# Performance work log

Measured on AMD Instinct MI355X. Metric: run time of the kernel, lower is better.

Reference implementation:

```python
import jax, jax.numpy as jnp
import numpy as np

H = 2; C = 64          # heads, hidden_channels
N = 50000; E = 800000  # nodes, edges
D = 128                # input_dim
EPS = 1e-5

def _lrelu(x, s):
    return jnp.where(x >= 0, x, s * x)

def _ln(x, g, b):
    m = x.mean(-1, keepdims=True)
    v = ((x - m) ** 2).mean(-1, keepdims=True)
    return (x - m) / jnp.sqrt(v + EPS) * g + b

def _gatv2(x_src, x_dst, src, dst, Wl, bl, Wr, br, att, Wres, bias):
    # PyG GATv2Conv: concat=False (mean over heads), residual=True, no self loops
    n = x_dst.shape[0]
    xl = (x_src @ Wl + bl).reshape(-1, H, C)  # [Ns,H,C]
    xr = (x_dst @ Wr + br).reshape(-1, H, C)  # [Nd,H,C]
    xj = xl[src]                               # [E,H,C] messages from source
    xi = xr[dst]                               # [E,H,C]
    e = _lrelu(xi + xj, 0.2)
    alpha = jnp.einsum('ehc,hc->eh', e, att)   # [E,H]
    amax = jax.lax.stop_gradient(jax.ops.segment_max(alpha, dst, num_segments=n))
    ex = jnp.exp(alpha - amax[dst])
    den = jax.ops.segment_sum(ex, dst, num_segments=n)
    a = ex / den[dst]                          # segment softmax over incoming edges
    out = jax.ops.segment_sum(xj * a[:, :, None], dst, num_segments=n)  # [Nd,H,C]
    return out.mean(axis=1) + x_dst @ Wres + bias


def setup_inputs() -> dict:
    key = jax.random.key(0)
    ks = jax.random.split(key, 40)
    d = {}
    d['x'] = jax.random.normal(ks[0], (N, D), jnp.float32)
    d['edge_index'] = jax.random.randint(ks[1], (2, E), 0, N, jnp.int32)
    i = 2
    for p, ind in (('c1d', D), ('c1t', D), ('c2d', C), ('c2t', C)):
        d[p + '_Wl'] = jax.random.normal(ks[i], (ind, H * C), jnp.float32) * 0.05; i += 1
        d[p + '_bl'] = jnp.zeros((H * C,), jnp.float32)
        d[p + '_Wr'] = jax.random.normal(ks[i], (ind, H * C), jnp.float32) * 0.05; i += 1
        d[p + '_br'] = jnp.zeros((H * C,), jnp.float32)
        d[p + '_att'] = jax.random.normal(ks[i], (H, C), jnp.float32) * 0.05; i += 1
        d[p + '_Wres'] = jax.random.normal(ks[i], (ind, C), jnp.float32) * 0.05; i += 1
        d[p + '_bias'] = jnp.zeros((C,), jnp.float32)
    d['nd_g'] = jnp.ones((C,), jnp.float32); d['nd_b'] = jnp.zeros((C,), jnp.float32)
    d['nt_g'] = jnp.ones((C,), jnp.float32); d['nt_b'] = jnp.zeros((C,), jnp.float32)
    return d


def reference(x, edge_index, c1d_Wl, c1d_bl, c1d_Wr, c1d_br, c1d_att, c1d_Wres, c1d_bias, c1t_Wl, c1t_bl, c1t_Wr, c1t_br, c1t_att, c1t_Wres, c1t_bias, c2d_Wl, c2d_bl, c2d_Wr, c2d_br, c2d_att, c2d_Wres, c2d_bias, c2t_Wl, c2t_bl, c2t_Wr, c2t_br, c2t_att, c2t_Wres, c2t_bias, nd_g, nd_b, nt_g, nt_b):
    src, dst = edge_index[0], edge_index[1]
    dep = _gatv2(x, x, src, dst, c1d_Wl, c1d_bl, c1d_Wr, c1d_br, c1d_att, c1d_Wres, c1d_bias)
    dep = _lrelu(_ln(dep, nd_g, nd_b), 0.01)
    dant = _gatv2(x, x, dst, src, c1t_Wl, c1t_bl, c1t_Wr, c1t_br, c1t_att, c1t_Wres, c1t_bias)
    dant = _lrelu(_ln(dant, nt_g, nt_b), 0.01)
    dep2 = _lrelu(_gatv2(dep, dep, src, dst, c2d_Wl, c2d_bl, c2d_Wr, c2d_br, c2d_att, c2d_Wres, c2d_bias), 0.01)
    dant2 = _lrelu(_gatv2(dant, dant, dst, src, c2t_Wl, c2t_bl, c2t_Wr, c2t_br, c2t_att, c2t_Wres, c2t_bias), 0.01)
    return jnp.concatenate([dep2, dant2, x], axis=-1)
```

## Files before the change

### kernel.cpp

```cpp
#include <hip/hip_runtime.h>
#include <math.h>

typedef unsigned short ushort_t;
typedef __attribute__((ext_vector_type(8))) short short8x;
typedef __attribute__((ext_vector_type(4))) float f32x4;

#define SUBS 8
#define CAP 128

__device__ __forceinline__ unsigned f2bf(float f) {
  unsigned u = __float_as_uint(f);
  u += 0x7fff + ((u >> 16) & 1);
  return u >> 16;
}
__device__ __forceinline__ float bf2f(ushort_t u) {
  return __uint_as_float(((unsigned)u) << 16);
}
__device__ __forceinline__ float dpp_red8(float v) {
  v += __int_as_float(__builtin_amdgcn_update_dpp(0, __float_as_int(v), 0xB1, 0xF, 0xF, true));
  v += __int_as_float(__builtin_amdgcn_update_dpp(0, __float_as_int(v), 0x4E, 0xF, 0xF, true));
  v += __int_as_float(__builtin_amdgcn_update_dpp(0, __float_as_int(v), 0x141, 0xF, 0xF, true));
  return v;
}

struct GArgs {
  const float* Wl[2];
  const float* bl[2];
  const float* Wr[2];
  const float* br[2];
  const float* Wres[2];
  const float* bias[2];
};

__device__ __forceinline__ float wval1(const GArgs& ga, int col, int k) {
  int dir = col >= 320 ? 1 : 0;
  int cc = col - dir * 320;
  return cc < 128 ? ga.Wl[dir][k * 128 + cc]
       : cc < 256 ? ga.Wr[dir][k * 128 + (cc - 128)]
                  : ga.Wres[dir][k * 64 + (cc - 256)];
}
__device__ __forceinline__ float bval(const GArgs& ga, int col) {
  int dir = col >= 320 ? 1 : 0;
  int cc = col - dir * 320;
  return cc < 128 ? ga.bl[dir][cc]
       : cc < 256 ? ga.br[dir][cc - 128]
                  : ga.bias[dir][cc - 256];
}


__global__ __launch_bounds__(128) void pack_kernel(GArgs g1, GArgs g2,
                                                   ushort_t* __restrict__ WT1,
                                                   ushort_t* __restrict__ WT2,
                                                   float* __restrict__ bc1,
                                                   float* __restrict__ bc2) {
  int b = blockIdx.x;
  int k = threadIdx.x;
  if (b < 640) {
    WT1[b * 128 + k] = (ushort_t)f2bf(wval1(g1, b, k));
  } else if (b < 1280) {
    int c = b - 640;
    int dir = c >= 320 ? 1 : 0;
    int cc = c - dir * 320;
    float v = 0.f;
    if ((k >> 6) == dir) {
      int k2 = k & 63;
      v = cc < 128 ? g2.Wl[dir][k2 * 128 + cc]
        : cc < 256 ? g2.Wr[dir][k2 * 128 + (cc - 128)]
                   : g2.Wres[dir][k2 * 64 + (cc - 256)];
    }
    WT2[c * 128 + k] = (ushort_t)f2bf(v);
  } else {
    for (int c = k; c < 640; c += 128) {
      bc1[c] = bval(g1, c);
      bc2[c] = bval(g2, c);
    }
  }
}


template <int AF32>
__device__ __forceinline__ void gemm_body(const float* Af, const ushort_t* Ab,
                                          const ushort_t* WT, const float* bc,
                                          ushort_t* Y, int N, int rb, int cb,
                                          ushort_t* lds) {
  const int tid = threadIdx.x;
  const int lane = tid & 63;
  const int w = tid >> 6;
  const int m0 = rb * 64;
  const int cbase = cb * 128 + w * 32;

#pragma unroll
  for (int c = 0; c < 4; ++c) {
    int Lb = (tid + c * 256) * 16;
    int row = Lb >> 8, within = Lb & 255;
    int so = within ^ ((row & 7) << 4);
    int grow = m0 + row;
    if (grow >= N) grow = N - 1;
    if (AF32) {
      const float* src = Af + (size_t)grow * 128 + (so >> 1);
      float4 a = *(const float4*)src;
      float4 b = *(const float4*)(src + 4);
      uint4 o;
      o.x = f2bf(a.x) | (f2bf(a.y) << 16);
      o.y = f2bf(a.z) | (f2bf(a.w) << 16);
      o.z = f2bf(b.x) | (f2bf(b.y) << 16);
      o.w = f2bf(b.z) | (f2bf(b.w) << 16);
      ((uint4*)lds)[tid + c * 256] = o;
    } else {
      ((uint4*)lds)[tid + c * 256] = *(const uint4*)(Ab + (size_t)grow * 128 + (so >> 1));
    }
  }

  short8x bf[4][2];
#pragma unroll
  for (int ks = 0; ks < 4; ++ks)
#pragma unroll
    for (int ns = 0; ns < 2; ++ns) {
      int col = cbase + ns * 16 + (lane & 15);
      bf[ks][ns] = *(const short8x*)(WT + (size_t)col * 128 + ks * 32 + (lane >> 4) * 8);
    }

  __syncthreads();

  f32x4 z = {0.f, 0.f, 0.f, 0.f};
  f32x4 acc[4][2];
#pragma unroll
  for (int ms = 0; ms < 4; ++ms) {
    acc[ms][0] = z;
    acc[ms][1] = z;
  }
#pragma unroll
  for (int ks = 0; ks < 4; ++ks) {
    short8x af[4];
#pragma unroll
    for (int ms = 0; ms < 4; ++ms) {
      int row = ms * 16 + (lane & 15);
      int byte = row * 256 + ((ks * 64 + (lane >> 4) * 16) ^ ((row & 7) << 4));
      af[ms] = *(const short8x*)((const char*)lds + byte);
    }
#pragma unroll
    for (int ms = 0; ms < 4; ++ms) {
      acc[ms][0] = __builtin_amdgcn_mfma_f32_16x16x32_bf16(af[ms], bf[ks][0], acc[ms][0], 0, 0, 0);
      acc[ms][1] = __builtin_amdgcn_mfma_f32_16x16x32_bf16(af[ms], bf[ks][1], acc[ms][1], 0, 0, 0);
    }
  }

#pragma unroll
  for (int ms = 0; ms < 4; ++ms)
#pragma unroll
    for (int ns = 0; ns < 2; ++ns) {
      int col = cbase + ns * 16 + (lane & 15);
      float bv = bc[col];
#pragma unroll
      for (int r = 0; r < 4; ++r) {
        int grow = m0 + ms * 16 + (lane >> 4) * 4 + r;
        if (grow < N) Y[(size_t)grow * 640 + col] = (ushort_t)f2bf(acc[ms][ns][r] + bv);
      }
    }
}


__global__ __launch_bounds__(256) void k_front(
    const float* __restrict__ x, const int* __restrict__ ei, int E, int N,
    int* __restrict__ st0, int* __restrict__ st1, int* __restrict__ cnt0,
    int* __restrict__ cnt1, const ushort_t* __restrict__ WT1,
    const float* __restrict__ bc1, ushort_t* __restrict__ Y,
    float* __restrict__ out, int nbin, int ngemm, int nrow) {
  __shared__ ushort_t lds[8192];
  const int bid = blockIdx.x;
  const int t = threadIdx.x;
  if (bid < nbin) {
    const int sub = bid & (SUBS - 1);
    const int i0 = (bid * 256 + t) * 4;
    if (i0 >= E) return;
    if (i0 + 3 < E && (E & 3) == 0) {
      int4 sv = *(const int4*)(ei + i0);
      int4 dv = *(const int4*)(ei + E + i0);
      int ss[4] = {sv.x, sv.y, sv.z, sv.w};
      int dd[4] = {dv.x, dv.y, dv.z, dv.w};
      int pos[8], tgt[8];
#pragma unroll
      for (int j = 0; j < 4; ++j) {
        int c0 = (dd[j] >> 5) * SUBS + sub;
        tgt[j] = c0 * CAP;
        pos[j] = atomicAdd(&cnt0[c0], 1);
      }
#pragma unroll
      for (int j = 0; j < 4; ++j) {
        int c1 = (ss[j] >> 5) * SUBS + sub;
        tgt[4 + j] = c1 * CAP;
        pos[4 + j] = atomicAdd(&cnt1[c1], 1);
      }
#pragma unroll
      for (int j = 0; j < 4; ++j)
        if (pos[j] < CAP) st0[tgt[j] + pos[j]] = (ss[j] << 5) | (dd[j] & 31);
#pragma unroll
      for (int j = 0; j < 4; ++j)
        if (pos[4 + j] < CAP) st1[tgt[4 + j] + pos[4 + j]] = (dd[j] << 5) | (ss[j] & 31);
    } else {
      for (int i = i0; i < min(i0 + 4, E); ++i) {
        int s = ei[i], d = ei[E + i];
        int c0 = (d >> 5) * SUBS + sub;
        int i_ = atomicAdd(&cnt0[c0], 1);
        if (i_ < CAP) st0[c0 * CAP + i_] = (s << 5) | (d & 31);
        int c1 = (s >> 5) * SUBS + sub;
        int j_ = atomicAdd(&cnt1[c1], 1);
        if (j_ < CAP) st1[c1 * CAP + j_] = (d << 5) | (s & 31);
      }
    }
  } else if (bid < nbin + ngemm) {
    int gb = bid - nbin;
    gemm_body<1>(x, nullptr, WT1, bc1, Y, N, gb % nrow, gb / nrow, lds);
  } else {
    int i = (bid - nbin - ngemm) * 256 + t;
    if (i < N * 32) {
      float4 v = ((const float4*)x)[i];
      ((float4*)out)[(size_t)(i >> 5) * 64 + 32 + (i & 31)] = v;
    }
  }
}


__global__ __launch_bounds__(256) void gemm2_kernel(const ushort_t* __restrict__ A,
                                                    const ushort_t* __restrict__ WT,
                                                    const float* __restrict__ bc,
                                                    ushort_t* __restrict__ Y, int N) {
  __shared__ ushort_t lds[8192];
  gemm_body<0>(nullptr, A, WT, bc, Y, N, blockIdx.x, blockIdx.y, lds);
}


template <int MODE>
__global__ __launch_bounds__(256) void agg_bucket(
    const ushort_t* __restrict__ Y, const int* __restrict__ st0,
    const int* __restrict__ st1, const int* __restrict__ cnt0,
    const int* __restrict__ cnt1, const float* __restrict__ attA,
    const float* __restrict__ attB, const float* __restrict__ lng0,
    const float* __restrict__ lnb0, const float* __restrict__ lng1,
    const float* __restrict__ lnb1, void* __restrict__ outp, int N) {
  __shared__ int lnbr[SUBS * CAP + 8];
  __shared__ int hist[32], offs[32], cur[32];
  __shared__ int csub[SUBS + 1];
  const int b = blockIdx.x;
  const int dir = blockIdx.y;
  const int t = threadIdx.x;
  const int* st = dir ? st1 : st0;
  const int* cnt = dir ? cnt1 : cnt0;
  const float* att = dir ? attB : attA;

  for (int i = t; i < SUBS * CAP + 8; i += 256) lnbr[i] = 0;
  if (t < 32) {
    hist[t] = 0;
    cur[t] = 0;
  }
  if (t == 64) {
    int a = 0;
    for (int s = 0; s < SUBS; ++s) {
      csub[s] = a;
      a += min(cnt[b * SUBS + s], CAP);
    }
    csub[SUBS] = a;
  }
  __syncthreads();
#pragma unroll
  for (int s = 0; s < SUBS; ++s) {
    int base = csub[s], c = csub[s + 1] - base;
    for (int i = t; i < c; i += 256)
      atomicAdd(&hist[st[(b * SUBS + s) * CAP + i] & 31], 1);
  }
  __syncthreads();
  if (t < 32) {
    int v = hist[t], inc = v;
#pragma unroll
    for (int o = 1; o < 32; o <<= 1) {
      int u = __shfl_up(inc, o);
      if (t >= o) inc += u;
    }
    offs[t] = inc - v;
  }
  __syncthreads();
#pragma unroll
  for (int s = 0; s < SUBS; ++s) {
    int base = csub[s], c = csub[s + 1] - base;
    for (int i = t; i < c; i += 256) {
      int e = st[(b * SUBS + s) * CAP + i];
      int r = e & 31;
      lnbr[offs[r] + atomicAdd(&cur[r], 1)] = (int)((unsigned)e >> 5) * 1280;
    }
  }
  __syncthreads();

  const int wv = t >> 6, lane = t & 63, g = lane >> 4, jj = lane & 15;
  const float L2E = 1.4426950408889634f;
  float av[8];
  {
    float4 a0 = *(const float4*)(att + jj * 8);
    float4 a1 = *(const float4*)(att + jj * 8 + 4);
    av[0] = a0.x * L2E; av[1] = a0.y * L2E; av[2] = a0.z * L2E; av[3] = a0.w * L2E;
    av[4] = a1.x * L2E; av[5] = a1.y * L2E; av[6] = a1.z * L2E; av[7] = a1.w * L2E;
  }
  const char* Yb = (const char*)Y + dir * 640 + jj * 16;

  for (int r = wv; r < 32; r += 4) {
    const int n = b * 32 + r;
    if (n >= N) break;
    const char* rowp = (const char*)Y + (size_t)n * 1280 + dir * 640;

    float xi[8];
    {
      short8x v = *(const short8x*)(rowp + 256 + jj * 16);
#pragma unroll
      for (int q = 0; q < 8; ++q) xi[q] = bf2f((ushort_t)v[q]);
    }
    float d = 0.f;
    float acc[8];
#pragma unroll
    for (int q = 0; q < 8; ++q) acc[q] = 0.f;

    const int beg = offs[r], deg = hist[r];
    if (deg > 0) {
      int off = lnbr[beg + g];
      short8x vj = *(const short8x*)(Yb + (size_t)(unsigned)off);
      for (int k0 = 0; k0 < deg; k0 += 4) {
        int offn = lnbr[beg + k0 + 4 + g];
        short8x vn = *(const short8x*)(Yb + (size_t)(unsigned)offn);
        float xj[8];
#pragma unroll
        for (int q = 0; q < 8; ++q) xj[q] = bf2f((ushort_t)vj[q]);
        float p = 0.f;
#pragma unroll
        for (int q = 0; q < 8; ++q) {
          float e = xi[q] + xj[q];
          e = fmaxf(e, 0.2f * e);
          p = fmaf(e, av[q], p);
        }
        p = dpp_red8(p);
        float wgt = (k0 + g < deg) ? __builtin_amdgcn_exp2f(p) : 0.f;
        d += wgt;
#pragma unroll
        for (int q = 0; q < 8; ++q) acc[q] = fmaf(xj[q], wgt, acc[q]);
        vj = vn;
      }
#pragma unroll
      for (int o = 16; o <= 32; o <<= 1) {
        d += __shfl_xor(d, o);
#pragma unroll
        for (int q = 0; q < 8; ++q) acc[q] += __shfl_xor(acc[q], o);
      }
    }
    float inv = deg > 0 ? 1.f / d : 0.f;
    float v[8];
#pragma unroll
    for (int q = 0; q < 8; ++q) {
      float tq = acc[q] * inv;
      v[q] = 0.5f * (tq + __shfl_xor(tq, 8));
    }
    {
      short8x rv = *(const short8x*)(rowp + 512 + (jj & 7) * 16);
#pragma unroll
      for (int q = 0; q < 8; ++q) v[q] += bf2f((ushort_t)rv[q]);
    }

    if (MODE == 0) {
      float s = 0.f;
#pragma unroll
      for (int q = 0; q < 8; ++q) s += v[q];
      s += __shfl_xor(s, 1);
      s += __shfl_xor(s, 2);
      s += __shfl_xor(s, 4);
      float mu = s * (1.f / 64.f);
      float vs = 0.f;
#pragma unroll
      for (int q = 0; q < 8; ++q) {
        float dv = v[q] - mu;
        vs += dv * dv;
      }
      vs += __shfl_xor(vs, 1);
      vs += __shfl_xor(vs, 2);
      vs += __shfl_xor(vs, 4);
      float rstd = rsqrtf(vs * (1.f / 64.f) + 1e-5f);
      if (g == 0 && jj < 8) {
        const float* lg = dir ? lng1 : lng0;
        const float* lb = dir ? lnb1 : lnb0;
        unsigned o2[8];
#pragma unroll
        for (int q = 0; q < 8; ++q) {
          int c = jj * 8 + q;
          float y = (v[q] - mu) * rstd * lg[c] + lb[c];
          y = fmaxf(y, 0.01f * y);
          o2[q] = f2bf(y);
        }
        uint4 pk;
        pk.x = o2[0] | (o2[1] << 16);
        pk.y = o2[2] | (o2[3] << 16);
        pk.z = o2[4] | (o2[5] << 16);
        pk.w = o2[6] | (o2[7] << 16);
        *(uint4*)((ushort_t*)outp + (size_t)n * 128 + dir * 64 + jj * 8) = pk;
      }
    } else {
      if (g == 0 && jj < 8) {
        float* op = (float*)outp + (size_t)n * 256 + dir * 64 + jj * 8;
        float4 o0, o1;
        o0.x = fmaxf(v[0], 0.01f * v[0]);
        o0.y = fmaxf(v[1], 0.01f * v[1]);
        o0.z = fmaxf(v[2], 0.01f * v[2]);
        o0.w = fmaxf(v[3], 0.01f * v[3]);
        o1.x = fmaxf(v[4], 0.01f * v[4]);
        o1.y = fmaxf(v[5], 0.01f * v[5]);
        o1.z = fmaxf(v[6], 0.01f * v[6]);
        o1.w = fmaxf(v[7], 0.01f * v[7]);
        *(float4*)op = o0;
        *(float4*)(op + 4) = o1;
      }
    }
  }
}


extern "C" void kernel_launch(void* const* d_in, const int* in_sizes, int n_in,
                              void* d_out, int out_size, void* d_ws, size_t ws_size,
                              hipStream_t stream) {
  const float* x = (const float*)d_in[0];
  const int* ei = (const int*)d_in[1];
  const int N = in_sizes[0] / 128;
  const int E = in_sizes[1] / 2;
  float* out = (float*)d_out;
  const int nbuck = (N + 31) >> 5;

  char* p = (char*)d_ws;
  auto carve = [&](size_t bytes) {
    char* q = p;
    p += ((bytes + 255) & ~(size_t)255);
    return q;
  };
  int* cnt = (int*)carve((size_t)2 * nbuck * SUBS * 4);
  int* st0 = (int*)carve((size_t)nbuck * SUBS * CAP * 4);
  int* st1 = (int*)carve((size_t)nbuck * SUBS * CAP * 4);
  ushort_t* Y1 = (ushort_t*)carve((size_t)N * 640 * 2);
  ushort_t* A2 = (ushort_t*)carve((size_t)N * 128 * 2);
  ushort_t* WT1 = (ushort_t*)carve(640 * 128 * 2);
  ushort_t* WT2 = (ushort_t*)carve(640 * 128 * 2);
  float* bc1 = (float*)carve(640 * 4);
  float* bc2 = (float*)carve(640 * 4);
  int* cnt0 = cnt;
  int* cnt1 = cnt + (size_t)nbuck * SUBS;

  auto F = [&](int i) { return (const float*)d_in[i]; };
  GArgs g1, g2;
  g1.Wl[0] = F(2);  g1.bl[0] = F(3);  g1.Wr[0] = F(4);  g1.br[0] = F(5);
  g1.Wres[0] = F(7); g1.bias[0] = F(8);
  g1.Wl[1] = F(9);  g1.bl[1] = F(10); g1.Wr[1] = F(11); g1.br[1] = F(12);
  g1.Wres[1] = F(14); g1.bias[1] = F(15);
  g2.Wl[0] = F(16); g2.bl[0] = F(17); g2.Wr[0] = F(18); g2.br[0] = F(19);
  g2.Wres[0] = F(21); g2.bias[0] = F(22);
  g2.Wl[1] = F(23); g2.bl[1] = F(24); g2.Wr[1] = F(25); g2.br[1] = F(26);
  g2.Wres[1] = F(28); g2.bias[1] = F(29);

  hipMemsetAsync(cnt, 0, (size_t)2 * nbuck * SUBS * 4, stream);

  pack_kernel<<<1281, 128, 0, stream>>>(g1, g2, WT1, WT2, bc1, bc2);

  const int nbin = (E + 1023) / 1024;
  const int nrow = (N + 63) / 64;
  const int ngemm = nrow * 5;
  const int ncopy = (N * 32 + 255) / 256;
  k_front<<<nbin + ngemm + ncopy, 256, 0, stream>>>(
      x, ei, E, N, st0, st1, cnt0, cnt1, WT1, bc1, Y1, out, nbin, ngemm, nrow);

  const dim3 ga(nbuck, 2);
  agg_bucket<0><<<ga, 256, 0, stream>>>(Y1, st0, st1, cnt0, cnt1, F(6), F(13),
                                        F(30), F(31), F(32), F(33), A2, N);
  gemm2_kernel<<<dim3(nrow, 5), 256, 0, stream>>>(A2, WT2, bc2, Y1, N);
  agg_bucket<1><<<ga, 256, 0, stream>>>(Y1, st0, st1, cnt0, cnt1, F(20), F(27),
                                        nullptr, nullptr, nullptr, nullptr, out, N);
}
```

Before: 339.1 us.

## Replace fine-grained atomic edge binning with coarse LDS-histogram chunk binning

Edge binning now groups edges into 512-node coarse chunks. Each block builds LDS histograms and reserves space with one global atomic per chunk, instead of one global atomic per edge into 32-node sub-buckets. Aggregation blocks then scan their whole coarse chunk, filter the edges for their own 32 nodes into LDS, and sort them locally. This cuts contended global atomics in the front kernel. In exchange, each coarse chunk's edge list is read 16 times over in each aggregation pass, and endpoints are packed into 16-bit fields, which assumes fewer than 65536 nodes.

New measurement: 305.8 us. 1.11x faster.

```diff
diff --git a/kernel.cpp b/kernel.cpp
--- a/kernel.cpp
+++ b/kernel.cpp
@@ -5,8 +5,11 @@
 typedef __attribute__((ext_vector_type(8))) short short8x;
 typedef __attribute__((ext_vector_type(4))) float f32x4;
 
-#define SUBS 8
-#define CAP 128
+#define CSHIFT 9
+#define CC 12288
+#define EPB 4096
+#define ECAP 1024
+#define NCMAX 128
 
 __device__ __forceinline__ unsigned f2bf(float f) {
   unsigned u = __float_as_uint(f);
@@ -162,57 +165,53 @@
 
 __global__ __launch_bounds__(256) void k_front(
     const float* __restrict__ x, const int* __restrict__ ei, int E, int N,
-    int* __restrict__ st0, int* __restrict__ st1, int* __restrict__ cnt0,
-    int* __restrict__ cnt1, const ushort_t* __restrict__ WT1,
+    int* __restrict__ gc0, int* __restrict__ gc1, int* __restrict__ ctail0,
+    int* __restrict__ ctail1, const ushort_t* __restrict__ WT1,
     const float* __restrict__ bc1, ushort_t* __restrict__ Y,
-    float* __restrict__ out, int nbin, int ngemm, int nrow) {
+    float* __restrict__ out, int nbinA, int ngemm, int nrow) {
   __shared__ ushort_t lds[8192];
   const int bid = blockIdx.x;
   const int t = threadIdx.x;
-  if (bid < nbin) {
-    const int sub = bid & (SUBS - 1);
-    const int i0 = (bid * 256 + t) * 4;
-    if (i0 >= E) return;
-    if (i0 + 3 < E && (E & 3) == 0) {
-      int4 sv = *(const int4*)(ei + i0);
-      int4 dv = *(const int4*)(ei + E + i0);
-      int ss[4] = {sv.x, sv.y, sv.z, sv.w};
-      int dd[4] = {dv.x, dv.y, dv.z, dv.w};
-      int pos[8], tgt[8];
-#pragma unroll
-      for (int j = 0; j < 4; ++j) {
-        int c0 = (dd[j] >> 5) * SUBS + sub;
-        tgt[j] = c0 * CAP;
-        pos[j] = atomicAdd(&cnt0[c0], 1);
-      }
-#pragma unroll
-      for (int j = 0; j < 4; ++j) {
-        int c1 = (ss[j] >> 5) * SUBS + sub;
-        tgt[4 + j] = c1 * CAP;
-        pos[4 + j] = atomicAdd(&cnt1[c1], 1);
-      }
-#pragma unroll
-      for (int j = 0; j < 4; ++j)
-        if (pos[j] < CAP) st0[tgt[j] + pos[j]] = (ss[j] << 5) | (dd[j] & 31);
-#pragma unroll
-      for (int j = 0; j < 4; ++j)
-        if (pos[4 + j] < CAP) st1[tgt[4 + j] + pos[4 + j]] = (dd[j] << 5) | (ss[j] & 31);
-    } else {
-      for (int i = i0; i < min(i0 + 4, E); ++i) {
-        int s = ei[i], d = ei[E + i];
-        int c0 = (d >> 5) * SUBS + sub;
-        int i_ = atomicAdd(&cnt0[c0], 1);
-        if (i_ < CAP) st0[c0 * CAP + i_] = (s << 5) | (d & 31);
-        int c1 = (s >> 5) * SUBS + sub;
-        int j_ = atomicAdd(&cnt1[c1], 1);
-        if (j_ < CAP) st1[c1 * CAP + j_] = (d << 5) | (s & 31);
-      }
-    }
-  } else if (bid < nbin + ngemm) {
-    int gb = bid - nbin;
+  if (bid < nbinA) {
+    int* h0 = (int*)lds;
+    int* h1 = h0 + NCMAX;
+    int* b0 = h1 + NCMAX;
+    int* b1 = b0 + NCMAX;
+    const int e0 = bid * EPB;
+    const int e1 = min(e0 + EPB, E);
+    for (int i = t; i < NCMAX; i += 256) {
+      h0[i] = 0;
+      h1[i] = 0;
+    }
+    __syncthreads();
+    for (int i = e0 + t; i < e1; i += 256) {
+      int s = ei[i], d = ei[E + i];
+      atomicAdd(&h0[d >> CSHIFT], 1);
+      atomicAdd(&h1[s >> CSHIFT], 1);
+    }
+    __syncthreads();
+    for (int c = t; c < NCMAX; c += 256) {
+      int n0 = h0[c], n1 = h1[c];
+      b0[c] = n0 ? atomicAdd(&ctail0[c], n0) : 0;
+      b1[c] = n1 ? atomicAdd(&ctail1[c], n1) : 0;
+      h0[c] = 0;
+      h1[c] = 0;
+    }
+    __syncthreads();
+    for (int i = e0 + t; i < e1; i += 256) {
+      int s = ei[i], d = ei[E + i];
+      int c0 = d >> CSHIFT;
+      int p0 = b0[c0] + atomicAdd(&h0[c0], 1);
+      if (p0 < CC) gc0[c0 * CC + p0] = (s << 16) | d;
+      int c1 = s >> CSHIFT;
+      int p1 = b1[c1] + atomicAdd(&h1[c1], 1);
+      if (p1 < CC) gc1[c1 * CC + p1] = (d << 16) | s;
+    }
+  } else if (bid < nbinA + ngemm) {
+    int gb = bid - nbinA;
     gemm_body<1>(x, nullptr, WT1, bc1, Y, N, gb % nrow, gb / nrow, lds);
   } else {
-    int i = (bid - nbin - ngemm) * 256 + t;
+    int i = (bid - nbinA - ngemm) * 256 + t;
     if (i < N * 32) {
       float4 v = ((const float4*)x)[i];
       ((float4*)out)[(size_t)(i >> 5) * 64 + 32 + (i & 31)] = v;
@@ -232,42 +231,46 @@
 
 template <int MODE>
 __global__ __launch_bounds__(256) void agg_bucket(
-    const ushort_t* __restrict__ Y, const int* __restrict__ st0,
-    const int* __restrict__ st1, const int* __restrict__ cnt0,
-    const int* __restrict__ cnt1, const float* __restrict__ attA,
+    const ushort_t* __restrict__ Y, const int* __restrict__ gc0,
+    const int* __restrict__ gc1, const int* __restrict__ ctail0,
+    const int* __restrict__ ctail1, const float* __restrict__ attA,
     const float* __restrict__ attB, const float* __restrict__ lng0,
     const float* __restrict__ lnb0, const float* __restrict__ lng1,
     const float* __restrict__ lnb1, void* __restrict__ outp, int N) {
-  __shared__ int lnbr[SUBS * CAP + 8];
+  __shared__ int ebuf[ECAP];
+  __shared__ int lnbr[ECAP + 8];
   __shared__ int hist[32], offs[32], cur[32];
-  __shared__ int csub[SUBS + 1];
-  const int b = blockIdx.x;
+  __shared__ int ecnt;
+  const int fb = blockIdx.x;
+  const int cb = fb >> 4;
   const int dir = blockIdx.y;
   const int t = threadIdx.x;
-  const int* st = dir ? st1 : st0;
-  const int* cnt = dir ? cnt1 : cnt0;
+  const int* gc = dir ? gc1 : gc0;
+  const int* ctail = dir ? ctail1 : ctail0;
   const float* att = dir ? attB : attA;
 
-  for (int i = t; i < SUBS * CAP + 8; i += 256) lnbr[i] = 0;
+  for (int i = t; i < ECAP + 8; i += 256) lnbr[i] = 0;
   if (t < 32) {
     hist[t] = 0;
     cur[t] = 0;
   }
-  if (t == 64) {
-    int a = 0;
-    for (int s = 0; s < SUBS; ++s) {
-      csub[s] = a;
-      a += min(cnt[b * SUBS + s], CAP);
-    }
-    csub[SUBS] = a;
-  }
-  __syncthreads();
-#pragma unroll
-  for (int s = 0; s < SUBS; ++s) {
-    int base = csub[s], c = csub[s + 1] - base;
-    for (int i = t; i < c; i += 256)
-      atomicAdd(&hist[st[(b * SUBS + s) * CAP + i] & 31], 1);
-  }
+  if (t == 64) ecnt = 0;
+  __syncthreads();
+
+  {
+    const int cntc = min(ctail[cb], CC);
+    const int* src = gc + cb * CC;
+    for (int i = t; i < cntc; i += 256) {
+      int e = src[i];
+      if (((e & 0xFFFF) >> 5) == fb) {
+        int idx = atomicAdd(&ecnt, 1);
+        if (idx < ECAP) ebuf[idx] = e;
+      }
+    }
+  }
+  __syncthreads();
+  const int tot = min(ecnt, ECAP);
+  for (int i = t; i < tot; i += 256) atomicAdd(&hist[ebuf[i] & 31], 1);
   __syncthreads();
   if (t < 32) {
     int v = hist[t], inc = v;
@@ -279,14 +282,10 @@
     offs[t] = inc - v;
   }
   __syncthreads();
-#pragma unroll
-  for (int s = 0; s < SUBS; ++s) {
-    int base = csub[s], c = csub[s + 1] - base;
-    for (int i = t; i < c; i += 256) {
-      int e = st[(b * SUBS + s) * CAP + i];
-      int r = e & 31;
-      lnbr[offs[r] + atomicAdd(&cur[r], 1)] = (int)((unsigned)e >> 5) * 1280;
-    }
+  for (int i = t; i < tot; i += 256) {
+    int e = ebuf[i];
+    int r = e & 31;
+    lnbr[offs[r] + atomicAdd(&cur[r], 1)] = (int)((unsigned)e >> 16) * 1280;
   }
   __syncthreads();
 
@@ -302,7 +301,7 @@
   const char* Yb = (const char*)Y + dir * 640 + jj * 16;
 
   for (int r = wv; r < 32; r += 4) {
-    const int n = b * 32 + r;
+    const int n = fb * 32 + r;
     if (n >= N) break;
     const char* rowp = (const char*)Y + (size_t)n * 1280 + dir * 640;
 
@@ -426,6 +425,7 @@
   const int E = in_sizes[1] / 2;
   float* out = (float*)d_out;
   const int nbuck = (N + 31) >> 5;
+  const int ncoarse = (N + (1 << CSHIFT) - 1) >> CSHIFT;
 
   char* p = (char*)d_ws;
   auto carve = [&](size_t bytes) {
@@ -433,17 +433,17 @@
     p += ((bytes + 255) & ~(size_t)255);
     return q;
   };
-  int* cnt = (int*)carve((size_t)2 * nbuck * SUBS * 4);
-  int* st0 = (int*)carve((size_t)nbuck * SUBS * CAP * 4);
-  int* st1 = (int*)carve((size_t)nbuck * SUBS * CAP * 4);
+  int* ctail = (int*)carve(2 * NCMAX * 4);
+  int* gc0 = (int*)carve((size_t)ncoarse * CC * 4);
+  int* gc1 = (int*)carve((size_t)ncoarse * CC * 4);
   ushort_t* Y1 = (ushort_t*)carve((size_t)N * 640 * 2);
   ushort_t* A2 = (ushort_t*)carve((size_t)N * 128 * 2);
   ushort_t* WT1 = (ushort_t*)carve(640 * 128 * 2);
   ushort_t* WT2 = (ushort_t*)carve(640 * 128 * 2);
   float* bc1 = (float*)carve(640 * 4);
   float* bc2 = (float*)carve(640 * 4);
-  int* cnt0 = cnt;
-  int* cnt1 = cnt + (size_t)nbuck * SUBS;
+  int* ctail0 = ctail;
+  int* ctail1 = ctail + NCMAX;
 
   auto F = [&](int i) { return (const float*)d_in[i]; };
   GArgs g1, g2;
@@ -456,21 +456,22 @@
   g2.Wl[1] = F(23); g2.bl[1] = F(24); g2.Wr[1] = F(25); g2.br[1] = F(26);
   g2.Wres[1] = F(28); g2.bias[1] = F(29);
 
-  hipMemsetAsync(cnt, 0, (size_t)2 * nbuck * SUBS * 4, stream);
+  hipMemsetAsync(ctail, 0, 2 * NCMAX * 4, stream);
 
   pack_kernel<<<1281, 128, 0, stream>>>(g1, g2, WT1, WT2, bc1, bc2);
 
-  const int nbin = (E + 1023) / 1024;
+  const int nbinA = (E + EPB - 1) / EPB;
   const int nrow = (N + 63) / 64;
   const int ngemm = nrow * 5;
   const int ncopy = (N * 32 + 255) / 256;
-  k_front<<<nbin + ngemm + ncopy, 256, 0, stream>>>(
-      x, ei, E, N, st0, st1, cnt0, cnt1, WT1, bc1, Y1, out, nbin, ngemm, nrow);
+  k_front<<<nbinA + ngemm + ncopy, 256, 0, stream>>>(
+      x, ei, E, N, gc0, gc1, ctail0, ctail1, WT1, bc1, Y1, out,
+      nbinA, ngemm, nrow);
 
   const dim3 ga(nbuck, 2);
-  agg_bucket<0><<<ga, 256, 0, stream>>>(Y1, st0, st1, cnt0, cnt1, F(6), F(13),
+  agg_bucket<0><<<ga, 256, 0, stream>>>(Y1, gc0, gc1, ctail0, ctail1, F(6), F(13),
                                         F(30), F(31), F(32), F(33), A2, N);
   gemm2_kernel<<<dim3(nrow, 5), 256, 0, stream>>>(A2, WT2, bc2, Y1, N);
-  agg_bucket<1><<<ga, 256, 0, stream>>>(Y1, st0, st1, cnt0, cnt1, F(20), F(27),
+  agg_bucket<1><<<ga, 256, 0, stream>>>(Y1, gc0, gc1, ctail0, ctail1, F(20), F(27),
                                         nullptr, nullptr, nullptr, nullptr, out, N);
 }
```
